# Kernel optimization log

Hardware: AMD Instinct MI355X
Metric: run time of the kernel (lower is better)

Reference implementation:

```python
import jax, jax.numpy as jnp
import numpy as np

B, EC, D = 16, 8192, 512   # batch, E*capacity, d_model
E, F = 8, 2048             # num_local_experts, d_ff
C = EC // E                # capacity per expert


def setup_inputs() -> dict:
    key = jax.random.key(0)
    k0, k1, k2 = jax.random.split(key, 3)
    inputs = jax.random.normal(k0, (B, EC, D), dtype=jnp.float32)
    # Stacked per-expert FFN parameters (expert e owns w1[e], b1[e], w2[e], b2[e]).
    w1 = jax.random.normal(k1, (E, D, F), dtype=jnp.float32) * (1.0 / np.sqrt(D))
    b1 = jnp.zeros((E, F), dtype=jnp.float32)
    w2 = jax.random.normal(k2, (E, F, D), dtype=jnp.float32) * (1.0 / np.sqrt(F))
    b2 = jnp.zeros((E, D), dtype=jnp.float32)
    return {"inputs": inputs, "w1": w1, "b1": b1, "w2": w2, "b2": b2}


def reference(inputs, w1, b1, w2, b2):
    # Original: chunk dim=1 into E pieces, run expert_e on chunk e, concat on dim=1.
    # Equivalent batched form: reshape dim 1 -> (E, C) and do grouped GEMMs.
    x = inputs.reshape(B, E, C, D)
    h = jnp.einsum('becd,edf->becf', x, w1) + b1[None, :, None, :]
    h = jax.nn.gelu(h)
    y = jnp.einsum('becf,efd->becd', h, w2) + b2[None, :, None, :]
    return y.reshape(B, EC, D)
```

## Files before the change

kernel.cpp:

```cpp
#include <hip/hip_runtime.h>
#include <hip/hip_bf16.h>
#include <stdint.h>

typedef __attribute__((ext_vector_type(8))) short short8;
typedef __attribute__((ext_vector_type(4))) float floatx4;

namespace {

constexpr int  BB  = 16;
constexpr int  E_  = 8;
constexpr int  CAP = 1024;
constexpr int  D_  = 512;
constexpr int  F_  = 2048;
constexpr long EC_ = (long)E_ * CAP;
constexpr long M_  = (long)BB * CAP;

constexpr int BM = 128, BN = 128, BK = 32;

static_assert(M_ % BM == 0 && F_ % BN == 0 && D_ % BN == 0, "tile divisibility");
static_assert(D_ % BK == 0 && F_ % BK == 0, "K divisibility");

__device__ __forceinline__ float gelu_tanh(float x) {
    const float k0 = 0.7978845608028654f;
    const float k1 = 0.044715f;
    float u = k0 * x * (1.0f + k1 * x * x);
    float t = 1.0f - 2.0f / (__expf(2.0f * u) + 1.0f);
    return 0.5f * x * (1.0f + t);
}

template <int EPI>
__global__ __launch_bounds__(256, 2) void gemm_bt(
    const __hip_bfloat16* __restrict__ A,
    const __hip_bfloat16* __restrict__ Bt,
    const float* __restrict__ bias, void* __restrict__ Out,
    const int K, const int ldb, const int ldo,
    const long sAb, const long sAe,
    const long sBe, const int biasE,
    const long sOb, const long sOe)
{
    __shared__ __align__(16) __hip_bfloat16 As[BM * BK];
    __shared__ __align__(16) __hip_bfloat16 Bs[BN * BK];

    const int e  = blockIdx.z;
    const int m0 = blockIdx.y * BM;
    const int n0 = blockIdx.x * BN;

    const int tid  = threadIdx.x;
    const int wave = tid >> 6;
    const int lane = tid & 63;

    const int srow = lane >> 2;
    const int sk   = (lane & 3) * 8;

    const __hip_bfloat16* Ae = A  + (long)e * sAe;
    const __hip_bfloat16* Be = Bt + (long)e * sBe + (long)n0 * ldb;

    floatx4 acc[4][4] = {};

    const int wm = (wave >> 1) * 64;
    const int wn = (wave & 1) * 64;
    const int fr = lane & 15;
    const int fq = lane >> 4;

    for (int k0 = 0; k0 < K; k0 += BK) {
#pragma unroll
        for (int t = 0; t < 2; ++t) {
            const int ch = wave * 2 + t;
            const int mg = m0 + ch * 16 + srow;
            const int b  = mg >> 10;
            const int c  = mg & (CAP - 1);
            const __hip_bfloat16* gp = Ae + (long)b * sAb + (long)c * K + (k0 + sk);
            __builtin_amdgcn_global_load_lds(
                (const __attribute__((address_space(1))) void*)gp,
                (__attribute__((address_space(3))) void*)((char*)As + ch * 1024),
                16, 0, 0);
        }
#pragma unroll
        for (int t = 0; t < 2; ++t) {
            const int ch = wave * 2 + t;
            const int nr = ch * 16 + srow;
            const __hip_bfloat16* gp = Be + (long)nr * ldb + (k0 + sk);
            __builtin_amdgcn_global_load_lds(
                (const __attribute__((address_space(1))) void*)gp,
                (__attribute__((address_space(3))) void*)((char*)Bs + ch * 1024),
                16, 0, 0);
        }
        __syncthreads();

        short8 af[4], bf[4];
#pragma unroll
        for (int i = 0; i < 4; ++i)
            af[i] = *(const short8*)(As + (wm + i * 16 + fr) * BK + fq * 8);
#pragma unroll
        for (int j = 0; j < 4; ++j)
            bf[j] = *(const short8*)(Bs + (wn + j * 16 + fr) * BK + fq * 8);

#pragma unroll
        for (int i = 0; i < 4; ++i)
#pragma unroll
            for (int j = 0; j < 4; ++j)
                acc[i][j] = __builtin_amdgcn_mfma_f32_16x16x32_bf16(
                    af[i], bf[j], acc[i][j], 0, 0, 0);

        __syncthreads();
    }

#pragma unroll
    for (int j = 0; j < 4; ++j) {
        const int ng = n0 + wn + j * 16 + fr;
        const float bv = (EPI == 2) ? 0.0f : bias[(long)e * biasE + ng];
#pragma unroll
        for (int i = 0; i < 4; ++i) {
#pragma unroll
            for (int r = 0; r < 4; ++r) {
                const int mg = m0 + wm + i * 16 + fq * 4 + r;
                const int b  = mg >> 10;
                const int c  = mg & (CAP - 1);
                const long off = (long)b * sOb + (long)e * sOe + (long)c * ldo + ng;
                if (EPI == 0) {
                    ((__hip_bfloat16*)Out)[off] =
                        __float2bfloat16(gelu_tanh(acc[i][j][r] + bv));
                } else if (EPI == 1) {
                    ((float*)Out)[off] = acc[i][j][r] + bv;
                } else {
                    ((float*)Out)[off] += acc[i][j][r];
                }
            }
        }
    }
}

__global__ __launch_bounds__(256) void cvt_f32_bf16(
    const float* __restrict__ in, __hip_bfloat16* __restrict__ out, const long n)
{
    long i = ((long)blockIdx.x * blockDim.x + threadIdx.x) * 4;
    const long stride = (long)gridDim.x * blockDim.x * 4;
    for (; i < n; i += stride) {
        const float4 v = *(const float4*)(in + i);
        __hip_bfloat16 t0 = __float2bfloat16(v.x);
        __hip_bfloat16 t1 = __float2bfloat16(v.y);
        __hip_bfloat16 t2 = __float2bfloat16(v.z);
        __hip_bfloat16 t3 = __float2bfloat16(v.w);
        ushort4 o;
        o.x = *(unsigned short*)&t0;
        o.y = *(unsigned short*)&t1;
        o.z = *(unsigned short*)&t2;
        o.w = *(unsigned short*)&t3;
        *(ushort4*)(out + i) = o;
    }
}

__global__ __launch_bounds__(256) void transpose_cvt(
    const float* __restrict__ in, __hip_bfloat16* __restrict__ out,
    const int R, const int Cc)
{
    __shared__ float tile[32][33];
    const int e = blockIdx.z;
    const float* pin = in + (long)e * R * Cc;
    __hip_bfloat16* pout = out + (long)e * R * Cc;
    const int c0 = blockIdx.x * 32;
    const int r0 = blockIdx.y * 32;
    const int tx = threadIdx.x & 31;
    const int ty = threadIdx.x >> 5;
#pragma unroll
    for (int rr = ty; rr < 32; rr += 8)
        tile[rr][tx] = pin[(long)(r0 + rr) * Cc + c0 + tx];
    __syncthreads();
#pragma unroll
    for (int rr = ty; rr < 32; rr += 8)
        pout[(long)(c0 + rr) * R + r0 + tx] = __float2bfloat16(tile[tx][rr]);
}

}

extern "C" void kernel_launch(void* const* d_in, const int* in_sizes, int n_in,
                              void* d_out, int out_size, void* d_ws, size_t ws_size,
                              hipStream_t stream) {
    const float* x  = (const float*)d_in[0];
    const float* w1 = (const float*)d_in[1];
    const float* b1 = (const float*)d_in[2];
    const float* w2 = (const float*)d_in[3];
    const float* b2 = (const float*)d_in[4];
    float* out = (float*)d_out;

    const long nX  = (long)BB * EC_ * D_;
    const long nW1 = (long)E_ * D_ * F_;
    const long nW2 = nW1;

    __hip_bfloat16* xb  = (__hip_bfloat16*)d_ws;
    __hip_bfloat16* w1t = xb + nX;
    __hip_bfloat16* w2t = w1t + nW1;
    __hip_bfloat16* h   = w2t + nW2;

    const size_t fixed = (size_t)(nX + nW1 + nW2) * 2;

    int Fc = 0;
    for (int cand : {2048, 1024, 512, 256, 128}) {
        size_t need = fixed + (size_t)BB * EC_ * cand * 2;
        if (need <= ws_size) { Fc = cand; break; }
    }
    if (Fc == 0) return;

    cvt_f32_bf16<<<dim3(32768), dim3(256), 0, stream>>>(x, xb, nX);
    transpose_cvt<<<dim3(F_ / 32, D_ / 32, E_), dim3(256), 0, stream>>>(w1, w1t, D_, F_);
    transpose_cvt<<<dim3(D_ / 32, F_ / 32, E_), dim3(256), 0, stream>>>(w2, w2t, F_, D_);

    for (int f0 = 0; f0 < F_; f0 += Fc) {
        gemm_bt<0><<<dim3(Fc / BN, M_ / BM, E_), dim3(256), 0, stream>>>(
            xb, w1t + (long)f0 * D_, b1 + f0, h,
            D_, D_, Fc,
            EC_ * D_, (long)CAP * D_,
            (long)F_ * D_, F_,
            (long)E_ * CAP * Fc, (long)CAP * Fc);

        if (f0 == 0) {
            gemm_bt<1><<<dim3(D_ / BN, M_ / BM, E_), dim3(256), 0, stream>>>(
                h, w2t + f0, b2, out,
                Fc, F_, D_,
                (long)E_ * CAP * Fc, (long)CAP * Fc,
                (long)D_ * F_, D_,
                EC_ * D_, (long)CAP * D_);
        } else {
            gemm_bt<2><<<dim3(D_ / BN, M_ / BM, E_), dim3(256), 0, stream>>>(
                h, w2t + f0, nullptr, out,
                Fc, F_, D_,
                (long)E_ * CAP * Fc, (long)CAP * Fc,
                (long)D_ * F_, D_,
                EC_ * D_, (long)CAP * D_);
        }
    }
}
```

Baseline: 1.370 ms.

## Replace GEMM with 256x256 double-buffered, swizzled, 8-wave pipelined MFMA kernel

Replaces the 128x128x32 single-buffered GEMM with a 256x256x64 tile kernel using 512 threads and 128KB of dynamic LDS. Global-to-LDS loads are double-buffered and interleaved with four MFMA quarter-steps, with s_setprio and explicit waitcnt/barriers. It also XOR-swizzles LDS columns to avoid bank conflicts and remaps workgroup IDs across XCDs. Larger tiles raise data reuse and cut load stalls, at the cost of heavy LDS and register use, which may limit occupancy (launch_bounds still asks for 2 blocks per CU).

After: 1.170 ms. -14.6%, faster.

```diff
diff --git a/kernel.cpp b/kernel.cpp
--- a/kernel.cpp
+++ b/kernel.cpp
@@ -15,10 +15,11 @@
 constexpr long EC_ = (long)E_ * CAP;
 constexpr long M_  = (long)BB * CAP;
 
-constexpr int BM = 128, BN = 128, BK = 32;
-
-static_assert(M_ % BM == 0 && F_ % BN == 0 && D_ % BN == 0, "tile divisibility");
-static_assert(D_ % BK == 0 && F_ % BK == 0, "K divisibility");
+constexpr int BM = 256, BN = 256, BK = 64;
+constexpr int NT = 512;
+constexpr int LDSZ = 131072;
+
+static_assert(M_ % BM == 0 && D_ % BN == 0, "tile divisibility");
 
 __device__ __forceinline__ float gelu_tanh(float x) {
     const float k0 = 0.7978845608028654f;
@@ -28,8 +29,42 @@
     return 0.5f * x * (1.0f + t);
 }
 
+template <int I0, int J0>
+__device__ __forceinline__ void mfma_quad(floatx4 (&acc)[8][4],
+                                          const short8 (&af)[8],
+                                          const short8 (&bf)[4]) {
+#pragma unroll
+    for (int i = 0; i < 4; ++i)
+#pragma unroll
+        for (int j = 0; j < 2; ++j) {
+            floatx4 c = acc[I0 + i][J0 + j];
+            c = __builtin_amdgcn_mfma_f32_16x16x32_bf16(af[i * 2 + 0], bf[j * 2 + 0], c, 0, 0, 0);
+            c = __builtin_amdgcn_mfma_f32_16x16x32_bf16(af[i * 2 + 1], bf[j * 2 + 1], c, 0, 0, 0);
+            acc[I0 + i][J0 + j] = c;
+        }
+}
+
+#define STAGE_UNIT(U, TILE)                                                         \
+    do {                                                                            \
+        const int t_ = (TILE);                                                      \
+        if (t_ < nK) {                                                              \
+            const long ko_ = (long)t_ * (2 * BK);                                   \
+            char* const d_ = (((U) & 1) ? BsB : AsB) + (t_ & 1) * 32768 +           \
+                             ((U) >> 1) * 16384 + wv2 * 1024;                       \
+            const char* const gb_ = ((U) & 1) ? (const char*)Be : (const char*)Ae;  \
+            const int o0_ = ((U) & 1) ? boff[(U) >> 1][0] : aoff[(U) >> 1][0];      \
+            const int o1_ = ((U) & 1) ? boff[(U) >> 1][1] : aoff[(U) >> 1][1];      \
+            __builtin_amdgcn_global_load_lds(                                       \
+                (const __attribute__((address_space(1))) void*)(gb_ + o0_ + ko_),   \
+                (__attribute__((address_space(3))) void*)d_, 16, 0, 0);             \
+            __builtin_amdgcn_global_load_lds(                                       \
+                (const __attribute__((address_space(1))) void*)(gb_ + o1_ + ko_),   \
+                (__attribute__((address_space(3))) void*)(d_ + 1024), 16, 0, 0);    \
+        }                                                                           \
+    } while (0)
+
 template <int EPI>
-__global__ __launch_bounds__(256, 2) void gemm_bt(
+__global__ __launch_bounds__(NT, 2) void gemm8p(
     const __hip_bfloat16* __restrict__ A,
     const __hip_bfloat16* __restrict__ Bt,
     const float* __restrict__ bias, void* __restrict__ Out,
@@ -38,92 +73,159 @@
     const long sBe, const int biasE,
     const long sOb, const long sOe)
 {
-    __shared__ __align__(16) __hip_bfloat16 As[BM * BK];
-    __shared__ __align__(16) __hip_bfloat16 Bs[BN * BK];
-
-    const int e  = blockIdx.z;
-    const int m0 = blockIdx.y * BM;
-    const int n0 = blockIdx.x * BN;
-
-    const int tid  = threadIdx.x;
-    const int wave = tid >> 6;
+    extern __shared__ char smem[];
+    char* const AsB = smem;
+    char* const BsB = smem + 65536;
+
+    const int gx = (int)gridDim.x, gy = (int)gridDim.y;
+    const int nwg = gx * gy * (int)gridDim.z;
+    int id = (int)blockIdx.x + gx * ((int)blockIdx.y + gy * (int)blockIdx.z);
+    id = (id & 7) * (nwg >> 3) + (id >> 3);
+    const int nt = id % gx;
+    const int mt = (id / gx) % gy;
+    const int e  = id / (gx * gy);
+    const int m0 = mt * BM;
+    const int n0 = nt * BN;
+
+    const int tid  = (int)threadIdx.x;
     const int lane = tid & 63;
-
-    const int srow = lane >> 2;
-    const int sk   = (lane & 3) * 8;
-
-    const __hip_bfloat16* Ae = A  + (long)e * sAe;
-    const __hip_bfloat16* Be = Bt + (long)e * sBe + (long)n0 * ldb;
-
-    floatx4 acc[4][4] = {};
-
-    const int wm = (wave >> 1) * 64;
-    const int wn = (wave & 1) * 64;
-    const int fr = lane & 15;
-    const int fq = lane >> 4;
-
-    for (int k0 = 0; k0 < K; k0 += BK) {
+    const int w    = tid >> 6;
+    const int wv2  = w * 2;
+    const int wr   = w >> 2;
+    const int wc   = w & 3;
+    const int fr   = lane & 15;
+    const int fq   = lane >> 4;
+
+    const int nK = K >> 6;
+
+    const __hip_bfloat16* const Ae = A  + (long)e * sAe;
+    const __hip_bfloat16* const Be = Bt + (long)e * sBe + (long)n0 * ldb;
+
+    const int sk = ((lane & 7) ^ (lane >> 3)) << 3;
+    int aoff[2][2], boff[2][2];
+#pragma unroll
+    for (int half = 0; half < 2; ++half)
 #pragma unroll
         for (int t = 0; t < 2; ++t) {
-            const int ch = wave * 2 + t;
-            const int mg = m0 + ch * 16 + srow;
+            const int rit = half * 128 + (wv2 + t) * 8 + (lane >> 3);
+            const int mg  = m0 + rit;
+            const int b   = mg >> 10;
+            const int c   = mg & (CAP - 1);
+            aoff[half][t] = (int)(((long)b * sAb + (long)c * K + sk) * 2);
+            boff[half][t] = (int)(((long)rit * ldb + sk) * 2);
+        }
+
+    const int xm  = (fr & 7) << 4;
+    const int cb0 = (fq << 4) ^ xm;
+    const int cb1 = (64 | (fq << 4)) ^ xm;
+    const long rowA = (long)(wr * 128 + fr) * 128;
+    const long rowB = (long)(wc * 64 + fr) * 128;
+
+    floatx4 acc[8][4] = {};
+
+    STAGE_UNIT(0, 0); STAGE_UNIT(1, 0); STAGE_UNIT(2, 0); STAGE_UNIT(3, 0);
+    STAGE_UNIT(0, 1); STAGE_UNIT(1, 1);
+    if (nK >= 2) asm volatile("s_waitcnt vmcnt(4)" ::: "memory");
+    else         asm volatile("s_waitcnt vmcnt(0)" ::: "memory");
+    __builtin_amdgcn_s_barrier();
+    asm volatile("" ::: "memory");
+
+    for (int kt = 0; kt < nK; ++kt) {
+        const char* const asb = AsB + (kt & 1) * 32768 + rowA;
+        const char* const bsb = BsB + (kt & 1) * 32768 + rowB;
+        short8 a0[8], a1[8], b0[4], b1[4];
+
+#pragma unroll
+        for (int i = 0; i < 4; ++i) {
+            a0[i * 2 + 0] = *(const short8*)(asb + i * 2048 + cb0);
+            a0[i * 2 + 1] = *(const short8*)(asb + i * 2048 + cb1);
+        }
+#pragma unroll
+        for (int j = 0; j < 2; ++j) {
+            b0[j * 2 + 0] = *(const short8*)(bsb + j * 2048 + cb0);
+            b0[j * 2 + 1] = *(const short8*)(bsb + j * 2048 + cb1);
+        }
+        STAGE_UNIT(2, kt + 1);
+        __builtin_amdgcn_s_barrier();
+        asm volatile("s_waitcnt lgkmcnt(0)" ::: "memory");
+        __builtin_amdgcn_sched_barrier(0);
+        __builtin_amdgcn_s_setprio(1);
+        mfma_quad<0, 0>(acc, a0, b0);
+        __builtin_amdgcn_s_setprio(0);
+        __builtin_amdgcn_sched_barrier(0);
+        __builtin_amdgcn_s_barrier();
+        asm volatile("" ::: "memory");
+
+#pragma unroll
+        for (int i = 0; i < 4; ++i) {
+            a1[i * 2 + 0] = *(const short8*)(asb + (i + 4) * 2048 + cb0);
+            a1[i * 2 + 1] = *(const short8*)(asb + (i + 4) * 2048 + cb1);
+        }
+        STAGE_UNIT(3, kt + 1);
+        __builtin_amdgcn_s_barrier();
+        asm volatile("s_waitcnt lgkmcnt(0)" ::: "memory");
+        __builtin_amdgcn_sched_barrier(0);
+        __builtin_amdgcn_s_setprio(1);
+        mfma_quad<4, 0>(acc, a1, b0);
+        __builtin_amdgcn_s_setprio(0);
+        __builtin_amdgcn_sched_barrier(0);
+        __builtin_amdgcn_s_barrier();
+        asm volatile("" ::: "memory");
+
+#pragma unroll
+        for (int j = 0; j < 2; ++j) {
+            b1[j * 2 + 0] = *(const short8*)(bsb + (j + 2) * 2048 + cb0);
+            b1[j * 2 + 1] = *(const short8*)(bsb + (j + 2) * 2048 + cb1);
+        }
+        STAGE_UNIT(0, kt + 2);
+        __builtin_amdgcn_s_barrier();
+        asm volatile("s_waitcnt lgkmcnt(0)" ::: "memory");
+        __builtin_amdgcn_sched_barrier(0);
+        __builtin_amdgcn_s_setprio(1);
+        mfma_quad<0, 2>(acc, a0, b1);
+        __builtin_amdgcn_s_setprio(0);
+        __builtin_amdgcn_sched_barrier(0);
+        __builtin_amdgcn_s_barrier();
+        asm volatile("" ::: "memory");
+
+        STAGE_UNIT(1, kt + 2);
+        if (kt + 2 < nK) asm volatile("s_waitcnt vmcnt(4)" ::: "memory");
+        else             asm volatile("s_waitcnt vmcnt(0)" ::: "memory");
+        __builtin_amdgcn_s_barrier();
+        asm volatile("" ::: "memory");
+        __builtin_amdgcn_s_setprio(1);
+        mfma_quad<4, 2>(acc, a1, b1);
+        __builtin_amdgcn_s_setprio(0);
+        __builtin_amdgcn_s_barrier();
+        asm volatile("" ::: "memory");
+    }
+
+    float bv[4];
+#pragma unroll
+    for (int j = 0; j < 4; ++j) {
+        if constexpr (EPI != 2)
+            bv[j] = bias[(long)e * biasE + n0 + wc * 64 + j * 16 + fr];
+        else
+            bv[j] = 0.0f;
+    }
+#pragma unroll
+    for (int i = 0; i < 8; ++i) {
+#pragma unroll
+        for (int r = 0; r < 4; ++r) {
+            const int mg = m0 + wr * 128 + i * 16 + fq * 4 + r;
             const int b  = mg >> 10;
             const int c  = mg & (CAP - 1);
-            const __hip_bfloat16* gp = Ae + (long)b * sAb + (long)c * K + (k0 + sk);
-            __builtin_amdgcn_global_load_lds(
-                (const __attribute__((address_space(1))) void*)gp,
-                (__attribute__((address_space(3))) void*)((char*)As + ch * 1024),
-                16, 0, 0);
-        }
-#pragma unroll
-        for (int t = 0; t < 2; ++t) {
-            const int ch = wave * 2 + t;
-            const int nr = ch * 16 + srow;
-            const __hip_bfloat16* gp = Be + (long)nr * ldb + (k0 + sk);
-            __builtin_amdgcn_global_load_lds(
-                (const __attribute__((address_space(1))) void*)gp,
-                (__attribute__((address_space(3))) void*)((char*)Bs + ch * 1024),
-                16, 0, 0);
-        }
-        __syncthreads();
-
-        short8 af[4], bf[4];
-#pragma unroll
-        for (int i = 0; i < 4; ++i)
-            af[i] = *(const short8*)(As + (wm + i * 16 + fr) * BK + fq * 8);
-#pragma unroll
-        for (int j = 0; j < 4; ++j)
-            bf[j] = *(const short8*)(Bs + (wn + j * 16 + fr) * BK + fq * 8);
-
-#pragma unroll
-        for (int i = 0; i < 4; ++i)
-#pragma unroll
-            for (int j = 0; j < 4; ++j)
-                acc[i][j] = __builtin_amdgcn_mfma_f32_16x16x32_bf16(
-                    af[i], bf[j], acc[i][j], 0, 0, 0);
-
-        __syncthreads();
-    }
-
-#pragma unroll
-    for (int j = 0; j < 4; ++j) {
-        const int ng = n0 + wn + j * 16 + fr;
-        const float bv = (EPI == 2) ? 0.0f : bias[(long)e * biasE + ng];
-#pragma unroll
-        for (int i = 0; i < 4; ++i) {
-#pragma unroll
-            for (int r = 0; r < 4; ++r) {
-                const int mg = m0 + wm + i * 16 + fq * 4 + r;
-                const int b  = mg >> 10;
-                const int c  = mg & (CAP - 1);
-                const long off = (long)b * sOb + (long)e * sOe + (long)c * ldo + ng;
-                if (EPI == 0) {
-                    ((__hip_bfloat16*)Out)[off] =
-                        __float2bfloat16(gelu_tanh(acc[i][j][r] + bv));
-                } else if (EPI == 1) {
-                    ((float*)Out)[off] = acc[i][j][r] + bv;
+            const long ro = (long)b * sOb + (long)e * sOe + (long)c * ldo;
+#pragma unroll
+            for (int j = 0; j < 4; ++j) {
+                const int ng = n0 + wc * 64 + j * 16 + fr;
+                if constexpr (EPI == 0) {
+                    ((__hip_bfloat16*)Out)[ro + ng] =
+                        __float2bfloat16(gelu_tanh(acc[i][j][r] + bv[j]));
+                } else if constexpr (EPI == 1) {
+                    ((float*)Out)[ro + ng] = acc[i][j][r] + bv[j];
                 } else {
-                    ((float*)Out)[off] += acc[i][j][r];
+                    ((float*)Out)[ro + ng] += acc[i][j][r];
                 }
             }
         }
@@ -195,18 +297,29 @@
     const size_t fixed = (size_t)(nX + nW1 + nW2) * 2;
 
     int Fc = 0;
-    for (int cand : {2048, 1024, 512, 256, 128}) {
+    for (int cand : {2048, 1024, 512, 256}) {
         size_t need = fixed + (size_t)BB * EC_ * cand * 2;
         if (need <= ws_size) { Fc = cand; break; }
     }
     if (Fc == 0) return;
+
+    static bool attr_done = false;
+    if (!attr_done) {
+        hipFuncSetAttribute(reinterpret_cast<const void*>(&gemm8p<0>),
+                            hipFuncAttributeMaxDynamicSharedMemorySize, LDSZ);
+        hipFuncSetAttribute(reinterpret_cast<const void*>(&gemm8p<1>),
+                            hipFuncAttributeMaxDynamicSharedMemorySize, LDSZ);
+        hipFuncSetAttribute(reinterpret_cast<const void*>(&gemm8p<2>),
+                            hipFuncAttributeMaxDynamicSharedMemorySize, LDSZ);
+        attr_done = true;
+    }
 
     cvt_f32_bf16<<<dim3(32768), dim3(256), 0, stream>>>(x, xb, nX);
     transpose_cvt<<<dim3(F_ / 32, D_ / 32, E_), dim3(256), 0, stream>>>(w1, w1t, D_, F_);
     transpose_cvt<<<dim3(D_ / 32, F_ / 32, E_), dim3(256), 0, stream>>>(w2, w2t, F_, D_);
 
     for (int f0 = 0; f0 < F_; f0 += Fc) {
-        gemm_bt<0><<<dim3(Fc / BN, M_ / BM, E_), dim3(256), 0, stream>>>(
+        gemm8p<0><<<dim3(Fc / BN, (int)(M_ / BM), E_), dim3(NT), LDSZ, stream>>>(
             xb, w1t + (long)f0 * D_, b1 + f0, h,
             D_, D_, Fc,
             EC_ * D_, (long)CAP * D_,
@@ -214,14 +327,14 @@
             (long)E_ * CAP * Fc, (long)CAP * Fc);
 
         if (f0 == 0) {
-            gemm_bt<1><<<dim3(D_ / BN, M_ / BM, E_), dim3(256), 0, stream>>>(
+            gemm8p<1><<<dim3(D_ / BN, (int)(M_ / BM), E_), dim3(NT), LDSZ, stream>>>(
                 h, w2t + f0, b2, out,
                 Fc, F_, D_,
                 (long)E_ * CAP * Fc, (long)CAP * Fc,
                 (long)D_ * F_, D_,
                 EC_ * D_, (long)CAP * D_);
         } else {
-            gemm_bt<2><<<dim3(D_ / BN, M_ / BM, E_), dim3(256), 0, stream>>>(
+            gemm8p<2><<<dim3(D_ / BN, (int)(M_ / BM), E_), dim3(NT), LDSZ, stream>>>(
                 h, w2t + f0, nullptr, out,
                 Fc, F_, D_,
                 (long)E_ * CAP * Fc, (long)CAP * Fc,
```

## Double-buffer LDS with swizzled layout, wider 128x256 tiles and XCD-aware block remap

Applied to the files above, without the earlier changes.

The GEMM kernel now uses 128x256 tiles, so each wave computes a 64x128 sub-tile with 32 accumulators, which raises reuse of the A fragments. LDS is double-buffered so the global_load_lds for the next K-step is issued before the MFMAs of the current step, and only one barrier is taken per iteration. LDS columns are XOR-swizzled to reduce bank conflicts, and block ids are remapped in groups of 8, matching the 8 XCDs, to improve L2 locality. The cost is higher register pressure from 128 accumulator floats per lane and 48KB of LDS per block, which may reduce occupancy below the two blocks per CU requested.

After: 1.226 ms. 1.12x faster.

```diff
diff --git a/kernel.cpp b/kernel.cpp
--- a/kernel.cpp
+++ b/kernel.cpp
@@ -4,6 +4,9 @@
 
 typedef __attribute__((ext_vector_type(8))) short short8;
 typedef __attribute__((ext_vector_type(4))) float floatx4;
+
+typedef __attribute__((address_space(3))) char lds_char;
+typedef __attribute__((address_space(3))) const short8 lds_cshort8;
 
 namespace {
 
@@ -15,10 +18,10 @@
 constexpr long EC_ = (long)E_ * CAP;
 constexpr long M_  = (long)BB * CAP;
 
-constexpr int BM = 128, BN = 128, BK = 32;
-
-static_assert(M_ % BM == 0 && F_ % BN == 0 && D_ % BN == 0, "tile divisibility");
-static_assert(D_ % BK == 0 && F_ % BK == 0, "K divisibility");
+constexpr int BM = 128, BN = 256, BK = 32;
+constexpr int NT = 256;
+
+static_assert(M_ % BM == 0 && D_ % BN == 0, "tile divisibility");
 
 __device__ __forceinline__ float gelu_tanh(float x) {
     const float k0 = 0.7978845608028654f;
@@ -29,7 +32,7 @@
 }
 
 template <int EPI>
-__global__ __launch_bounds__(256, 2) void gemm_bt(
+__global__ __launch_bounds__(NT, 2) void gemm2p(
     const __hip_bfloat16* __restrict__ A,
     const __hip_bfloat16* __restrict__ Bt,
     const float* __restrict__ bias, void* __restrict__ Out,
@@ -38,96 +41,130 @@
     const long sBe, const int biasE,
     const long sOb, const long sOe)
 {
-    __shared__ __align__(16) __hip_bfloat16 As[BM * BK];
-    __shared__ __align__(16) __hip_bfloat16 Bs[BN * BK];
-
-    const int e  = blockIdx.z;
-    const int m0 = blockIdx.y * BM;
-    const int n0 = blockIdx.x * BN;
-
-    const int tid  = threadIdx.x;
-    const int wave = tid >> 6;
+    __shared__ __align__(16) __hip_bfloat16 smem[24576];
+    lds_char* const LA = (lds_char*)smem;
+    lds_char* const LBp = (lds_char*)smem + 16384;
+
+    const int gx = (int)gridDim.x, gy = (int)gridDim.y;
+    const int nwg = gx * gy * (int)gridDim.z;
+    int id = (int)blockIdx.x + gx * ((int)blockIdx.y + gy * (int)blockIdx.z);
+    id = (id & 7) * (nwg >> 3) + (id >> 3);
+    const int nt = id % gx;
+    const int mt = (id / gx) % gy;
+    const int e  = id / (gx * gy);
+    const int m0 = mt * BM;
+    const int n0 = nt * BN;
+
+    const int tid  = (int)threadIdx.x;
     const int lane = tid & 63;
-
-    const int srow = lane >> 2;
-    const int sk   = (lane & 3) * 8;
-
-    const __hip_bfloat16* Ae = A  + (long)e * sAe;
-    const __hip_bfloat16* Be = Bt + (long)e * sBe + (long)n0 * ldb;
-
-    floatx4 acc[4][4] = {};
-
-    const int wm = (wave >> 1) * 64;
-    const int wn = (wave & 1) * 64;
-    const int fr = lane & 15;
-    const int fq = lane >> 4;
-
-    for (int k0 = 0; k0 < K; k0 += BK) {
-#pragma unroll
-        for (int t = 0; t < 2; ++t) {
-            const int ch = wave * 2 + t;
-            const int mg = m0 + ch * 16 + srow;
-            const int b  = mg >> 10;
-            const int c  = mg & (CAP - 1);
-            const __hip_bfloat16* gp = Ae + (long)b * sAb + (long)c * K + (k0 + sk);
-            __builtin_amdgcn_global_load_lds(
-                (const __attribute__((address_space(1))) void*)gp,
-                (__attribute__((address_space(3))) void*)((char*)As + ch * 1024),
-                16, 0, 0);
-        }
-#pragma unroll
-        for (int t = 0; t < 2; ++t) {
-            const int ch = wave * 2 + t;
-            const int nr = ch * 16 + srow;
-            const __hip_bfloat16* gp = Be + (long)nr * ldb + (k0 + sk);
-            __builtin_amdgcn_global_load_lds(
-                (const __attribute__((address_space(1))) void*)gp,
-                (__attribute__((address_space(3))) void*)((char*)Bs + ch * 1024),
-                16, 0, 0);
-        }
-        __syncthreads();
-
-        short8 af[4], bf[4];
+    const int w    = tid >> 6;
+    const int wm   = (w >> 1) * 64;
+    const int wn   = (w & 1) * 128;
+    const int fr   = lane & 15;
+    const int fq   = lane >> 4;
+
+    const int nK = K >> 5;
+
+    const __hip_bfloat16* const Ae = A  + (long)e * sAe;
+    const __hip_bfloat16* const Be = Bt + (long)e * sBe + (long)n0 * ldb;
+
+    const int skB_ = ((lane & 3) ^ ((lane >> 3) & 3)) * 16;
+    const char* aP[2];
+    const char* bP[4];
+#pragma unroll
+    for (int t = 0; t < 2; ++t) {
+        const int ra = w * 32 + t * 16 + (lane >> 2);
+        const int mg = m0 + ra;
+        const int b  = mg >> 10;
+        const int c  = mg & (CAP - 1);
+        aP[t] = (const char*)Ae + ((long)b * sAb + (long)c * K) * 2 + skB_;
+    }
+#pragma unroll
+    for (int t = 0; t < 4; ++t) {
+        const int nr = w * 64 + t * 16 + (lane >> 2);
+        bP[t] = (const char*)Be + (long)nr * ldb * 2 + skB_;
+    }
+
+    const int cbr = (fq ^ ((fr >> 1) & 3)) << 4;
+
+#define STAGE(CB, KT)                                                              \
+    do {                                                                           \
+        if ((KT) < nK) {                                                           \
+            const long kb_ = (long)(KT) * 64;           \
+            _Pragma("unroll")                                                      \
+            for (int t = 0; t < 2; ++t)                                            \
+                __builtin_amdgcn_global_load_lds(                                  \
+                    (const __attribute__((address_space(1))) void*)(aP[t] + kb_),  \
+                    (__attribute__((address_space(3))) void*)(LA + (CB) * 8192 +   \
+                        w * 2048 + t * 1024), 16, 0, 0);                           \
+            _Pragma("unroll")                                                      \
+            for (int t = 0; t < 4; ++t)                                            \
+                __builtin_amdgcn_global_load_lds(                                  \
+                    (const __attribute__((address_space(1))) void*)(bP[t] + kb_),  \
+                    (__attribute__((address_space(3))) void*)(LBp + (CB) * 16384 + \
+                        w * 4096 + t * 1024), 16, 0, 0);                           \
+        }                                                                          \
+    } while (0)
+
+    floatx4 acc[4][8] = {};
+
+    STAGE(0, 0);
+    __syncthreads();
+
+    int c = 0;
+    for (int kt = 0; kt < nK; ++kt) {
+        STAGE(c ^ 1, kt + 1);
+
+        short8 af[4], bf[8];
 #pragma unroll
         for (int i = 0; i < 4; ++i)
-            af[i] = *(const short8*)(As + (wm + i * 16 + fr) * BK + fq * 8);
-#pragma unroll
-        for (int j = 0; j < 4; ++j)
-            bf[j] = *(const short8*)(Bs + (wn + j * 16 + fr) * BK + fq * 8);
+            af[i] = *(lds_cshort8*)(LA + c * 8192 + (wm + i * 16 + fr) * 64 + cbr);
+#pragma unroll
+        for (int j = 0; j < 8; ++j)
+            bf[j] = *(lds_cshort8*)(LBp + c * 16384 + (wn + j * 16 + fr) * 64 + cbr);
 
 #pragma unroll
         for (int i = 0; i < 4; ++i)
 #pragma unroll
-            for (int j = 0; j < 4; ++j)
+            for (int j = 0; j < 8; ++j)
                 acc[i][j] = __builtin_amdgcn_mfma_f32_16x16x32_bf16(
                     af[i], bf[j], acc[i][j], 0, 0, 0);
 
         __syncthreads();
-    }
-
-#pragma unroll
-    for (int j = 0; j < 4; ++j) {
-        const int ng = n0 + wn + j * 16 + fr;
-        const float bv = (EPI == 2) ? 0.0f : bias[(long)e * biasE + ng];
-#pragma unroll
-        for (int i = 0; i < 4; ++i) {
-#pragma unroll
-            for (int r = 0; r < 4; ++r) {
-                const int mg = m0 + wm + i * 16 + fq * 4 + r;
-                const int b  = mg >> 10;
-                const int c  = mg & (CAP - 1);
-                const long off = (long)b * sOb + (long)e * sOe + (long)c * ldo + ng;
-                if (EPI == 0) {
-                    ((__hip_bfloat16*)Out)[off] =
-                        __float2bfloat16(gelu_tanh(acc[i][j][r] + bv));
-                } else if (EPI == 1) {
-                    ((float*)Out)[off] = acc[i][j][r] + bv;
+        c ^= 1;
+    }
+
+    float bv[8];
+#pragma unroll
+    for (int j = 0; j < 8; ++j) {
+        if constexpr (EPI != 2)
+            bv[j] = bias[(long)e * biasE + n0 + wn + j * 16 + fr];
+        else
+            bv[j] = 0.0f;
+    }
+#pragma unroll
+    for (int i = 0; i < 4; ++i) {
+#pragma unroll
+        for (int r = 0; r < 4; ++r) {
+            const int mg = m0 + wm + i * 16 + fq * 4 + r;
+            const int b  = mg >> 10;
+            const int cc = mg & (CAP - 1);
+            const long ro = (long)b * sOb + (long)e * sOe + (long)cc * ldo;
+#pragma unroll
+            for (int j = 0; j < 8; ++j) {
+                const int ng = n0 + wn + j * 16 + fr;
+                if constexpr (EPI == 0) {
+                    ((__hip_bfloat16*)Out)[ro + ng] =
+                        __float2bfloat16(gelu_tanh(acc[i][j][r] + bv[j]));
+                } else if constexpr (EPI == 1) {
+                    ((float*)Out)[ro + ng] = acc[i][j][r] + bv[j];
                 } else {
-                    ((float*)Out)[off] += acc[i][j][r];
+                    ((float*)Out)[ro + ng] += acc[i][j][r];
                 }
             }
         }
     }
+#undef STAGE
 }
 
 __global__ __launch_bounds__(256) void cvt_f32_bf16(
@@ -195,7 +232,7 @@
     const size_t fixed = (size_t)(nX + nW1 + nW2) * 2;
 
     int Fc = 0;
-    for (int cand : {2048, 1024, 512, 256, 128}) {
+    for (int cand : {2048, 1024, 512, 256}) {
         size_t need = fixed + (size_t)BB * EC_ * cand * 2;
         if (need <= ws_size) { Fc = cand; break; }
     }
@@ -206,7 +243,7 @@
     transpose_cvt<<<dim3(D_ / 32, F_ / 32, E_), dim3(256), 0, stream>>>(w2, w2t, F_, D_);
 
     for (int f0 = 0; f0 < F_; f0 += Fc) {
-        gemm_bt<0><<<dim3(Fc / BN, M_ / BM, E_), dim3(256), 0, stream>>>(
+        gemm2p<0><<<dim3(Fc / BN, (int)(M_ / BM), E_), dim3(NT), 0, stream>>>(
             xb, w1t + (long)f0 * D_, b1 + f0, h,
             D_, D_, Fc,
             EC_ * D_, (long)CAP * D_,
@@ -214,14 +251,14 @@
             (long)E_ * CAP * Fc, (long)CAP * Fc);
 
         if (f0 == 0) {
-            gemm_bt<1><<<dim3(D_ / BN, M_ / BM, E_), dim3(256), 0, stream>>>(
+            gemm2p<1><<<dim3(D_ / BN, (int)(M_ / BM), E_), dim3(NT), 0, stream>>>(
                 h, w2t + f0, b2, out,
                 Fc, F_, D_,
                 (long)E_ * CAP * Fc, (long)CAP * Fc,
                 (long)D_ * F_, D_,
                 EC_ * D_, (long)CAP * D_);
         } else {
-            gemm_bt<2><<<dim3(D_ / BN, M_ / BM, E_), dim3(256), 0, stream>>>(
+            gemm2p<2><<<dim3(D_ / BN, (int)(M_ / BM), E_), dim3(NT), 0, stream>>>(
                 h, w2t + f0, nullptr, out,
                 Fc, F_, D_,
                 (long)E_ * CAP * Fc, (long)CAP * Fc,
```
